# Kernel tuning notes

Measured on AMD Instinct MI355X. Metric: run time of the kernel, lower is better.

Reference implementation:

```python
import jax, jax.numpy as jnp
import numpy as np

B, L, P, V, D = 8, 2048, 576, 32000, 2560
IGNORE_INDEX = -100
T = L - 1 + P  # image token removed, P patch embeddings spliced in


def setup_inputs() -> dict:
    key = jax.random.key(0)
    k1, k2, k3, k4, k5 = jax.random.split(key, 5)
    input_ids = jax.random.randint(k1, (B, L), 0, V, dtype=jnp.int32)
    # exactly one image-token position per sample (avoid first/last slot)
    img_pos = jax.random.randint(k2, (B,), 1, L - 2, dtype=jnp.int32)
    labels = jax.random.randint(k3, (B, L), 0, V, dtype=jnp.int32)
    embed_table = jax.random.normal(k4, (V, D), dtype=jnp.float32) * 0.02
    image_features = jax.random.normal(k5, (B, P, D), dtype=jnp.float32)
    return dict(embed_table=embed_table, image_features=image_features,
                input_ids=input_ids, labels=labels, img_pos=img_pos)


def reference(embed_table, image_features, input_ids, labels, img_pos):
    # Fused version of the per-sample splice loop:
    # out[b] = concat(embed(ids[b, :pos]), image_features[b], embed(ids[b, pos+1:]))
    tok_emb = embed_table[input_ids]                      # [B, L, D]
    j = jnp.arange(T, dtype=jnp.int32)[None, :]           # [1, T]
    pos = img_pos[:, None]                                # [B, 1]
    is_img = (j >= pos) & (j < pos + P)                   # [B, T]
    # token source index: before image -> j; after image -> skip img token
    tok_idx = jnp.clip(jnp.where(j < pos, j, j - P + 1), 0, L - 1)  # [B, T]
    img_idx = jnp.clip(j - pos, 0, P - 1)                 # [B, T]
    emb_tok = jnp.take_along_axis(tok_emb, tok_idx[..., None], axis=1)        # [B,T,D]
    emb_img = jnp.take_along_axis(image_features, img_idx[..., None], axis=1)  # [B,T,D]
    new_input_embeds = jnp.where(is_img[..., None], emb_img, emb_tok)
    lab_tok = jnp.take_along_axis(labels, tok_idx, axis=1)
    new_labels = jnp.where(is_img, jnp.int32(IGNORE_INDEX), lab_tok)
    attention_mask = jnp.ones((B, T), dtype=bool)
    position_ids = jnp.broadcast_to(jnp.arange(T, dtype=jnp.int32), (B, T))
    return new_input_embeds, new_labels, attention_mask, position_ids
```

## Files before the change

### kernel.cpp

```cpp
#include <hip/hip_runtime.h>

#define Bn 8
#define Ln 2048
#define Pn 576
#define Vn 32000
#define Dn 2560
#define Tn (Ln - 1 + Pn)
#define IGNORE_INDEX (-100)

__global__ __launch_bounds__(640) void splice_kernel(
    const float* __restrict__ embed_table,
    const float* __restrict__ image_features,
    const int*   __restrict__ input_ids,
    const int*   __restrict__ labels,
    const int*   __restrict__ img_pos,
    float* __restrict__ out)
{
    const int t = blockIdx.x;
    const int b = blockIdx.y;
    const int pos = img_pos[b];

    const bool is_img = (t >= pos) && (t < pos + Pn);

    const float4* __restrict__ src;
    int tok_idx = 0;
    if (is_img) {
        const int img_idx = t - pos;
        src = (const float4*)(image_features + ((size_t)b * Pn + img_idx) * Dn);
    } else {
        tok_idx = (t < pos) ? t : (t - Pn + 1);
        tok_idx = min(max(tok_idx, 0), Ln - 1);
        const int id = input_ids[b * Ln + tok_idx];
        src = (const float4*)(embed_table + (size_t)id * Dn);
    }

    float4* __restrict__ dst = (float4*)(out + ((size_t)b * Tn + t) * Dn);
    dst[threadIdx.x] = src[threadIdx.x];

    if (threadIdx.x == 0) {
        const size_t nBT  = (size_t)Bn * Tn;
        const size_t base = nBT * Dn;
        const size_t idx  = (size_t)b * Tn + t;
        float lab;
        if (is_img) {
            lab = (float)IGNORE_INDEX;
        } else {
            lab = (float)labels[b * Ln + tok_idx];
        }
        out[base + idx]            = lab;
        out[base + nBT + idx]      = 1.0f;
        out[base + 2 * nBT + idx]  = (float)t;
    }
}

extern "C" void kernel_launch(void* const* d_in, const int* in_sizes, int n_in,
                              void* d_out, int out_size, void* d_ws, size_t ws_size,
                              hipStream_t stream) {
    const float* embed_table    = (const float*)d_in[0];
    const float* image_features = (const float*)d_in[1];
    const int*   input_ids      = (const int*)d_in[2];
    const int*   labels         = (const int*)d_in[3];
    const int*   img_pos        = (const int*)d_in[4];
    float* out = (float*)d_out;

    dim3 grid(Tn, Bn);
    dim3 block(640);
    splice_kernel<<<grid, block, 0, stream>>>(embed_table, image_features,
                                              input_ids, labels, img_pos, out);
}
```

Before: 488.4 us.

## Switch splice copy to persistent wave-per-row loop with nontemporal loads/stores

Replaces the one-block-per-row launch with a grid-stride loop where each 64-lane wave copies a whole embedding row, ten float4 per lane, with all loads issued before the stores. Image-feature reads and all output writes use nontemporal hints so the streamed data stays out of the cache, while embedding-table reads stay cached for repeated token ids. The aim is to cut block scheduling overhead and raise memory-level parallelism on a purely bandwidth-bound gather copy. The fixed grid of 1312 blocks of 256 threads may leave some waves with one more row than others, so the work is slightly uneven.

Measured after the change: 498.1 us. About the same (+2.0%).

```diff
diff --git a/kernel.cpp b/kernel.cpp
--- a/kernel.cpp
+++ b/kernel.cpp
@@ -6,65 +6,86 @@
 #define Vn 32000
 #define Dn 2560
 #define Tn (Ln - 1 + Pn)
+#define NROWS (Bn * Tn)
 #define IGNORE_INDEX (-100)
+#define F4_PER_ROW (Dn / 4)
+#define F4_PER_LANE (F4_PER_ROW / 64)
 
-__global__ __launch_bounds__(640) void splice_kernel(
-    const float* __restrict__ embed_table,
-    const float* __restrict__ image_features,
-    const int*   __restrict__ input_ids,
-    const int*   __restrict__ labels,
-    const int*   __restrict__ img_pos,
+typedef float f4 __attribute__((ext_vector_type(4)));
+
+__global__ __launch_bounds__(256) void splice_kernel(
+    const f4* __restrict__ embed_table,
+    const f4* __restrict__ image_features,
+    const int* __restrict__ input_ids,
+    const int* __restrict__ labels,
+    const int* __restrict__ img_pos,
     float* __restrict__ out)
 {
-    const int t = blockIdx.x;
-    const int b = blockIdx.y;
-    const int pos = img_pos[b];
+    const int lane   = threadIdx.x & 63;
+    const int wave   = (int)((blockIdx.x * blockDim.x + threadIdx.x) >> 6);
+    const int nwaves = (int)((gridDim.x * blockDim.x) >> 6);
 
-    const bool is_img = (t >= pos) && (t < pos + Pn);
+    const size_t nBT = (size_t)NROWS;
+    float* __restrict__ extras = out + nBT * Dn;
 
-    const float4* __restrict__ src;
-    int tok_idx = 0;
-    if (is_img) {
-        const int img_idx = t - pos;
-        src = (const float4*)(image_features + ((size_t)b * Pn + img_idx) * Dn);
-    } else {
-        tok_idx = (t < pos) ? t : (t - Pn + 1);
-        tok_idx = min(max(tok_idx, 0), Ln - 1);
-        const int id = input_ids[b * Ln + tok_idx];
-        src = (const float4*)(embed_table + (size_t)id * Dn);
-    }
+    for (int row = wave; row < NROWS; row += nwaves) {
+        const int b = row / Tn;
+        const int t = row - b * Tn;
+        const int pos = img_pos[b];
 
-    float4* __restrict__ dst = (float4*)(out + ((size_t)b * Tn + t) * Dn);
-    dst[threadIdx.x] = src[threadIdx.x];
+        const bool is_img = (t >= pos) && (t < pos + Pn);
 
-    if (threadIdx.x == 0) {
-        const size_t nBT  = (size_t)Bn * Tn;
-        const size_t base = nBT * Dn;
-        const size_t idx  = (size_t)b * Tn + t;
-        float lab;
+        const f4* __restrict__ src;
+        int tok_idx = 0;
+        bool img_src = false;
         if (is_img) {
-            lab = (float)IGNORE_INDEX;
+            img_src = true;
+            src = image_features + ((size_t)b * Pn + (t - pos)) * F4_PER_ROW;
         } else {
-            lab = (float)labels[b * Ln + tok_idx];
+            tok_idx = (t < pos) ? t : (t - Pn + 1);
+            tok_idx = min(max(tok_idx, 0), Ln - 1);
+            const int id = input_ids[b * Ln + tok_idx];
+            src = embed_table + (size_t)id * F4_PER_ROW;
         }
-        out[base + idx]            = lab;
-        out[base + nBT + idx]      = 1.0f;
-        out[base + 2 * nBT + idx]  = (float)t;
+
+        f4* __restrict__ dst = (f4*)(out + (size_t)row * Dn);
+
+        f4 v[F4_PER_LANE];
+        if (img_src) {
+#pragma unroll
+            for (int k = 0; k < F4_PER_LANE; ++k)
+                v[k] = __builtin_nontemporal_load(src + lane + (k << 6));
+        } else {
+#pragma unroll
+            for (int k = 0; k < F4_PER_LANE; ++k)
+                v[k] = src[lane + (k << 6)];
+        }
+#pragma unroll
+        for (int k = 0; k < F4_PER_LANE; ++k)
+            __builtin_nontemporal_store(v[k], dst + lane + (k << 6));
+
+        if (lane == 0) {
+            const float lab = is_img ? (float)IGNORE_INDEX
+                                     : (float)labels[b * Ln + tok_idx];
+            extras[row]           = lab;
+            extras[nBT + row]     = 1.0f;
+            extras[2 * nBT + row] = (float)t;
+        }
     }
 }
 
 extern "C" void kernel_launch(void* const* d_in, const int* in_sizes, int n_in,
                               void* d_out, int out_size, void* d_ws, size_t ws_size,
                               hipStream_t stream) {
-    const float* embed_table    = (const float*)d_in[0];
-    const float* image_features = (const float*)d_in[1];
-    const int*   input_ids      = (const int*)d_in[2];
-    const int*   labels         = (const int*)d_in[3];
-    const int*   img_pos        = (const int*)d_in[4];
+    const f4* embed_table    = (const f4*)d_in[0];
+    const f4* image_features = (const f4*)d_in[1];
+    const int* input_ids     = (const int*)d_in[2];
+    const int* labels        = (const int*)d_in[3];
+    const int* img_pos       = (const int*)d_in[4];
     float* out = (float*)d_out;
 
-    dim3 grid(Tn, Bn);
-    dim3 block(640);
+    dim3 grid(1312);
+    dim3 block(256);
     splice_kernel<<<grid, block, 0, stream>>>(embed_table, image_features,
                                               input_ids, labels, img_pos, out);
 }
```
